# Kernel tuning notes

Measured on AMD Instinct MI355X. Metric: run time of the kernel, lower is better.

Reference implementation:

```python
import jax, jax.numpy as jnp
import numpy as np

B, N, D = 4, 4096, 1024


def setup_inputs() -> dict:
    key = jax.random.key(0)
    ks = jax.random.split(key, 7)
    s = 1.0 / np.sqrt(D)
    return {
        "x": jax.random.normal(ks[0], (B, N, D), dtype=jnp.float32),
        "Wq": jax.random.uniform(ks[1], (D, D), jnp.float32, -s, s),
        "bq": jax.random.uniform(ks[2], (D,), jnp.float32, -s, s),
        "Wk": jax.random.uniform(ks[3], (D, D), jnp.float32, -s, s),
        "bk": jax.random.uniform(ks[4], (D,), jnp.float32, -s, s),
        "Wv": jax.random.uniform(ks[5], (D, D), jnp.float32, -s, s),
        "bv": jax.random.uniform(ks[6], (D,), jnp.float32, -s, s),
    }


def reference(x, Wq, bq, Wk, bk, Wv, bv):
    # Projections (nn.Linear: x @ W.T + b; here W stored as [in, out])
    Q = x @ Wq + bq
    K = x @ Wk + bk
    V = x @ Wv + bv
    Qp = jax.nn.elu(Q) + 1.0  # positive feature map
    Kp = jax.nn.elu(K) + 1.0
    KV = jnp.einsum('bnd,bne->bde', Kp, V)          # [B, D, D]
    numerator = jnp.einsum('bnd,bde->bne', Qp, KV)  # [B, N, D]
    K_sum = Kp.sum(axis=1)                           # [B, D]
    norm = jnp.einsum('bnd,bd->bn', Qp, K_sum)[..., None]
    eps = 1e-6
    return numerator / (norm + eps)
```

## Files before the change

kernel.cpp:

```cpp
#include <hip/hip_runtime.h>
#include <hip/hip_bf16.h>
#include <cstdint>

typedef __bf16 bf16x8 __attribute__((ext_vector_type(8)));
typedef float  f32x4  __attribute__((ext_vector_type(4)));
typedef unsigned short u16x8 __attribute__((ext_vector_type(8)));

__device__ __forceinline__ unsigned short f2bf(float f) {
  __hip_bfloat16 h = __float2bfloat16(f);
  return __builtin_bit_cast(unsigned short, h);
}
__device__ __forceinline__ float bf2f(unsigned short u) {
  return __builtin_bit_cast(float, (unsigned)u << 16);
}

#define GL2LDS16(gp, lp)                                                      \
  __builtin_amdgcn_global_load_lds(                                           \
      (const __attribute__((address_space(1))) unsigned int*)(gp),            \
      (__attribute__((address_space(3))) unsigned int*)(lp), 16, 0, 0)

#define SBAR                                                                  \
  {                                                                           \
    __builtin_amdgcn_s_barrier();                                             \
    __builtin_amdgcn_sched_barrier(0);                                        \
  }
#define WAITV(n)                                                              \
  {                                                                           \
    asm volatile("s_waitcnt vmcnt(" #n ")" ::: "memory");                     \
    __builtin_amdgcn_sched_barrier(0);                                        \
  }
#define WAITL0                                                                \
  {                                                                           \
    asm volatile("s_waitcnt lgkmcnt(0)" ::: "memory");                        \
    __builtin_amdgcn_sched_barrier(0);                                        \
  }

template <int MODE>
__global__ __launch_bounds__(512, 2) void gemm256(
    const unsigned short* __restrict__ A, long long lda, long long aOffZ,
    const unsigned short* __restrict__ B, long long ldb, long long bOffZ,
    void* __restrict__ C, long long ldc, long long cOffZ,
    const float* __restrict__ bias, const float* __restrict__ norm,
    long long normOffZ, int K) {
  __shared__ __attribute__((aligned(16))) char lds[2 * 65536];
  const int t = threadIdx.x;
  const int wave = t >> 6, lane = t & 63;
  const int wm = wave >> 2, wn = wave & 3;
  const int fr = lane & 15, fq = lane >> 4;

  const int gx = gridDim.x, gy = gridDim.y;
  int flat = blockIdx.y * gx + blockIdx.x;
  const int total = gx * gy;
  if ((total & 7) == 0) flat = (flat & 7) * (total >> 3) + (flat >> 3);
  const int bx = flat % gx, by = flat / gx;
  const int m0 = by * 256, n0 = bx * 256;

  const long long z = blockIdx.z;
  long long aBase, bBase;
  if (MODE == 3) {
    const long long koff = (z & 3) * 4096 + (z >> 2) * 1024;
    aBase = koff;
    bBase = koff;
  } else if (MODE == 5) {
    aBase = (z >> 2) * 256;
    bBase = (z & 3) * 1048576ll + (z >> 2) * 256;
  } else {
    aBase = z * aOffZ;
    bBase = z * bOffZ;
  }
  const unsigned short* Az = A + aBase;
  const unsigned short* Bz = B + bBase;

  const unsigned short* gA[2];
  const unsigned short* gB[2];
#pragma unroll
  for (int c = 0; c < 2; ++c) {
    int d = c * 8192 + t * 16;
    int l = d ^ (((d >> 7) & 3) << 4);
    int row = l >> 6, kel = (l & 63) >> 1;
    gA[c] = Az + (long long)(m0 + row) * lda + kel;
    gB[c] = Bz + (long long)(n0 + row) * ldb + kel;
  }

  const int slotx = (fr >> 1) & 3;
  const int acore = wm * 8192 + fr * 64 + ((fq ^ slotx) << 4);
  const int bcore = wn * 4096 + fr * 64 + ((fq ^ slotx) << 4);

  f32x4 acc[8][4];
#pragma unroll
  for (int i = 0; i < 8; ++i)
#pragma unroll
    for (int j = 0; j < 4; ++j) acc[i][j] = (f32x4){0.f, 0.f, 0.f, 0.f};

  const int NT = K >> 6;

  auto stage_sub = [&](int tile, int which) {
    char* dst = lds + (tile & 1) * 65536 + which * 16384 + wave * 1024;
    const int kofs = (tile << 6) + ((which >> 1) << 5);
    if (which & 1) {
      GL2LDS16(gB[0] + kofs, dst);
      GL2LDS16(gB[1] + kofs, dst + 8192);
    } else {
      GL2LDS16(gA[0] + kofs, dst);
      GL2LDS16(gA[1] + kofs, dst + 8192);
    }
  };

  stage_sub(0, 0);
  stage_sub(0, 1);
  stage_sub(0, 2);
  stage_sub(0, 3);
  WAITV(4);
  SBAR;

  bf16x8 av[4], bv0[4], bv1[4];
  for (int tt = 0; tt < NT - 1; ++tt) {
    const char* bufp = lds + (tt & 1) * 65536;
#pragma unroll
    for (int i = 0; i < 4; ++i) {
      av[i] = *(const bf16x8*)(bufp + acore + i * 1024);
      bv0[i] = *(const bf16x8*)(bufp + 16384 + bcore + i * 1024);
    }
    stage_sub(tt + 1, 0);
    SBAR;
    WAITL0;
    __builtin_amdgcn_s_setprio(1);
#pragma unroll
    for (int mi = 0; mi < 4; ++mi)
#pragma unroll
      for (int ni = 0; ni < 4; ++ni)
        acc[mi][ni] = __builtin_amdgcn_mfma_f32_16x16x32_bf16(
            av[mi], bv0[ni], acc[mi][ni], 0, 0, 0);
    __builtin_amdgcn_s_setprio(0);
    SBAR;
#pragma unroll
    for (int i = 0; i < 4; ++i)
      av[i] = *(const bf16x8*)(bufp + acore + (4 + i) * 1024);
    stage_sub(tt + 1, 1);
    SBAR;
    WAITL0;
    __builtin_amdgcn_s_setprio(1);
#pragma unroll
    for (int mi = 0; mi < 4; ++mi)
#pragma unroll
      for (int ni = 0; ni < 4; ++ni)
        acc[4 + mi][ni] = __builtin_amdgcn_mfma_f32_16x16x32_bf16(
            av[mi], bv0[ni], acc[4 + mi][ni], 0, 0, 0);
    __builtin_amdgcn_s_setprio(0);
    WAITV(4);
    SBAR;
#pragma unroll
    for (int i = 0; i < 4; ++i) {
      av[i] = *(const bf16x8*)(bufp + 32768 + acore + i * 1024);
      bv1[i] = *(const bf16x8*)(bufp + 49152 + bcore + i * 1024);
    }
    stage_sub(tt + 1, 2);
    SBAR;
    WAITL0;
    __builtin_amdgcn_s_setprio(1);
#pragma unroll
    for (int mi = 0; mi < 4; ++mi)
#pragma unroll
      for (int ni = 0; ni < 4; ++ni)
        acc[mi][ni] = __builtin_amdgcn_mfma_f32_16x16x32_bf16(
            av[mi], bv1[ni], acc[mi][ni], 0, 0, 0);
    __builtin_amdgcn_s_setprio(0);
    SBAR;
#pragma unroll
    for (int i = 0; i < 4; ++i)
      av[i] = *(const bf16x8*)(bufp + 32768 + acore + (4 + i) * 1024);
    stage_sub(tt + 1, 3);
    SBAR;
    WAITL0;
    __builtin_amdgcn_s_setprio(1);
#pragma unroll
    for (int mi = 0; mi < 4; ++mi)
#pragma unroll
      for (int ni = 0; ni < 4; ++ni)
        acc[4 + mi][ni] = __builtin_amdgcn_mfma_f32_16x16x32_bf16(
            av[mi], bv1[ni], acc[4 + mi][ni], 0, 0, 0);
    __builtin_amdgcn_s_setprio(0);
    WAITV(4);
    SBAR;
  }

  {
    const char* bufp = lds + ((NT - 1) & 1) * 65536;
#pragma unroll
    for (int i = 0; i < 4; ++i) {
      av[i] = *(const bf16x8*)(bufp + acore + i * 1024);
      bv0[i] = *(const bf16x8*)(bufp + 16384 + bcore + i * 1024);
    }
    SBAR;
    WAITL0;
#pragma unroll
    for (int mi = 0; mi < 4; ++mi)
#pragma unroll
      for (int ni = 0; ni < 4; ++ni)
        acc[mi][ni] = __builtin_amdgcn_mfma_f32_16x16x32_bf16(
            av[mi], bv0[ni], acc[mi][ni], 0, 0, 0);
    SBAR;
#pragma unroll
    for (int i = 0; i < 4; ++i)
      av[i] = *(const bf16x8*)(bufp + acore + (4 + i) * 1024);
    SBAR;
    WAITL0;
#pragma unroll
    for (int mi = 0; mi < 4; ++mi)
#pragma unroll
      for (int ni = 0; ni < 4; ++ni)
        acc[4 + mi][ni] = __builtin_amdgcn_mfma_f32_16x16x32_bf16(
            av[mi], bv0[ni], acc[4 + mi][ni], 0, 0, 0);
    WAITV(0);
    SBAR;
#pragma unroll
    for (int i = 0; i < 4; ++i) {
      av[i] = *(const bf16x8*)(bufp + 32768 + acore + i * 1024);
      bv1[i] = *(const bf16x8*)(bufp + 49152 + bcore + i * 1024);
    }
    WAITL0;
#pragma unroll
    for (int mi = 0; mi < 4; ++mi)
#pragma unroll
      for (int ni = 0; ni < 4; ++ni)
        acc[mi][ni] = __builtin_amdgcn_mfma_f32_16x16x32_bf16(
            av[mi], bv1[ni], acc[mi][ni], 0, 0, 0);
#pragma unroll
    for (int i = 0; i < 4; ++i)
      av[i] = *(const bf16x8*)(bufp + 32768 + acore + (4 + i) * 1024);
    WAITL0;
#pragma unroll
    for (int mi = 0; mi < 4; ++mi)
#pragma unroll
      for (int ni = 0; ni < 4; ++ni)
        acc[4 + mi][ni] = __builtin_amdgcn_mfma_f32_16x16x32_bf16(
            av[mi], bv1[ni], acc[4 + mi][ni], 0, 0, 0);
  }

  const float* nrmz = (MODE == 4) ? (norm + z * normOffZ) : nullptr;
  float* Cf = (float*)C + z * cOffZ;
  unsigned short* Cu = (unsigned short*)C + z * cOffZ;
#pragma unroll
  for (int mi = 0; mi < 8; ++mi) {
    const int rbase = m0 + wm * 128 + mi * 16 + fq * 4;
    float nv[4];
#pragma unroll
    for (int j = 0; j < 4; ++j)
      if (MODE == 4) nv[j] = nrmz[rbase + j];
#pragma unroll
    for (int ni = 0; ni < 4; ++ni) {
      const int c = n0 + wn * 64 + ni * 16 + fr;
      float cb = 0.f;
      if (MODE == 0) cb = bias[c];
#pragma unroll
      for (int j = 0; j < 4; ++j) {
        float v = acc[mi][ni][j];
        if (MODE == 0) {
          v += cb;
          v = (v > 0.f) ? v + 1.f : __expf(v);
        }
        const long long ci = (long long)(rbase + j) * ldc + c;
        if (MODE == 4)
          Cf[ci] = v / nv[j];
        else
          Cu[ci] = f2bf(v);
      }
    }
  }
}

__global__ __launch_bounds__(256) void transpose_bf(
    const unsigned short* __restrict__ in, unsigned short* __restrict__ out) {
  __shared__ unsigned short tile[4096];
  const int t = threadIdx.x;
  const long long r0 = (long long)blockIdx.x * 64;
  const long long c0 = (long long)blockIdx.y * 64;
#pragma unroll
  for (int it = 0; it < 2; ++it) {
    const int id = it * 256 + t;
    const int r = id >> 3, cc = id & 7;
    const int pc = cc ^ ((r >> 3) & 7);
    *(u16x8*)&tile[r * 64 + pc * 8] =
        *(const u16x8*)&in[(r0 + r) * 1024 + c0 + cc * 8];
  }
  __syncthreads();
#pragma unroll
  for (int it = 0; it < 2; ++it) {
    const int id = it * 256 + t;
    const int c = id >> 3, r8 = (id & 7) * 8;
    const int pc = (c >> 3) ^ (r8 >> 3);
    u16x8 v;
#pragma unroll
    for (int j = 0; j < 8; ++j) v[j] = tile[(r8 + j) * 64 + pc * 8 + (c & 7)];
    *(u16x8*)&out[(c0 + c) * 16384 + r0 + r8] = v;
  }
}

__global__ __launch_bounds__(256) void reduce_kvt(
    const unsigned short* __restrict__ P, unsigned short* __restrict__ Out) {
  const long long i = ((long long)blockIdx.x * 256 + threadIdx.x) * 8;
  const int b = (int)(i >> 20);
  const long long ed = i & ((1ll << 20) - 1);
  float s[8] = {0.f, 0.f, 0.f, 0.f, 0.f, 0.f, 0.f, 0.f};
#pragma unroll
  for (int ks = 0; ks < 4; ++ks) {
    u16x8 v = *(const u16x8*)(P + ((long long)(ks * 4 + b) << 20) + ed);
#pragma unroll
    for (int j = 0; j < 8; ++j) s[j] += bf2f(v[j]);
  }
  u16x8 o;
#pragma unroll
  for (int j = 0; j < 8; ++j) o[j] = f2bf(s[j]);
  *(u16x8*)(Out + i) = o;
}

__global__ __launch_bounds__(256) void reduce_kvt_bias(
    const unsigned short* __restrict__ P, const float* __restrict__ bv,
    const float* __restrict__ Ksum, unsigned short* __restrict__ KVt) {
  const long long i = ((long long)blockIdx.x * 256 + threadIdx.x) * 8;
  const int b = (int)(i >> 20);
  const long long ed = i & ((1ll << 20) - 1);
  const int e = (int)(ed >> 10), d = (int)(ed & 1023);
  float s[8] = {0.f, 0.f, 0.f, 0.f, 0.f, 0.f, 0.f, 0.f};
#pragma unroll
  for (int ks = 0; ks < 4; ++ks) {
    u16x8 v = *(const u16x8*)(P + ((long long)(ks * 4 + b) << 20) + ed);
#pragma unroll
    for (int j = 0; j < 8; ++j) s[j] += bf2f(v[j]);
  }
  const float bve = bv[e];
  const float* kp = Ksum + b * 1024 + d;
  u16x8 o;
#pragma unroll
  for (int j = 0; j < 8; ++j) o[j] = f2bf(s[j] + bve * kp[j]);
  *(u16x8*)(KVt + i) = o;
}

__global__ __launch_bounds__(256) void transpose_w(
    const float* __restrict__ W, unsigned short* __restrict__ WT) {
  __shared__ float tile[32][33];
  const int tx = threadIdx.x & 31, ty = threadIdx.x >> 5;
  const int i0 = blockIdx.y * 32, o0 = blockIdx.x * 32;
#pragma unroll
  for (int s = 0; s < 32; s += 8)
    tile[ty + s][tx] = W[(long long)(i0 + ty + s) * 1024 + o0 + tx];
  __syncthreads();
#pragma unroll
  for (int s = 0; s < 32; s += 8)
    WT[(long long)(o0 + ty + s) * 1024 + i0 + tx] = f2bf(tile[tx][ty + s]);
}

__global__ __launch_bounds__(256) void convert_x(
    const float4* __restrict__ in, uint2* __restrict__ out, int n4) {
  const int stride = gridDim.x * blockDim.x;
  for (int i = blockIdx.x * blockDim.x + threadIdx.x; i < n4; i += stride) {
    float4 v = in[i];
    uint2 o;
    o.x = (unsigned)f2bf(v.x) | ((unsigned)f2bf(v.y) << 16);
    o.y = (unsigned)f2bf(v.z) | ((unsigned)f2bf(v.w) << 16);
    out[i] = o;
  }
}

__global__ __launch_bounds__(256) void ksum_kernel(
    const unsigned short* __restrict__ KpT, float* __restrict__ Ksum) {
  const int gw = (blockIdx.x * 256 + threadIdx.x) >> 6;
  const int lane = threadIdx.x & 63;
  const int d = gw >> 2, b = gw & 3;
  const unsigned short* p = KpT + (long long)d * 16384 + b * 4096 + lane * 8;
  float s = 0.f;
#pragma unroll
  for (int it = 0; it < 8; ++it) {
    u16x8 v = *(const u16x8*)(p + it * 512);
#pragma unroll
    for (int j = 0; j < 8; ++j) s += bf2f(v[j]);
  }
#pragma unroll
  for (int o = 32; o > 0; o >>= 1) s += __shfl_down(s, o, 64);
  if (lane == 0) Ksum[b * 1024 + d] = s;
}

__global__ __launch_bounds__(256) void norm_kernel(
    const unsigned short* __restrict__ Qp, const float* __restrict__ Ksum,
    float* __restrict__ nrm) {
  const int gw = (blockIdx.x * 256 + threadIdx.x) >> 6;
  const int lane = threadIdx.x & 63;
  const int b = gw >> 12;
  const unsigned short* q = Qp + (long long)gw * 1024 + lane * 8;
  const float* ks = Ksum + b * 1024 + lane * 8;
  float s = 0.f;
#pragma unroll
  for (int it = 0; it < 2; ++it) {
    u16x8 v = *(const u16x8*)(q + it * 512);
    float4 k0 = *(const float4*)(ks + it * 512);
    float4 k1 = *(const float4*)(ks + it * 512 + 4);
    s += bf2f(v[0]) * k0.x + bf2f(v[1]) * k0.y + bf2f(v[2]) * k0.z +
         bf2f(v[3]) * k0.w + bf2f(v[4]) * k1.x + bf2f(v[5]) * k1.y +
         bf2f(v[6]) * k1.z + bf2f(v[7]) * k1.w;
  }
#pragma unroll
  for (int o = 32; o > 0; o >>= 1) s += __shfl_down(s, o, 64);
  if (lane == 0) nrm[gw] = s + 1e-6f;
}

extern "C" void kernel_launch(void* const* d_in, const int* in_sizes, int n_in,
                              void* d_out, int out_size, void* d_ws,
                              size_t ws_size, hipStream_t stream) {
  const float* x  = (const float*)d_in[0];
  const float* Wq = (const float*)d_in[1];
  const float* bq = (const float*)d_in[2];
  const float* Wk = (const float*)d_in[3];
  const float* bk = (const float*)d_in[4];
  const float* Wv = (const float*)d_in[5];
  const float* bv = (const float*)d_in[6];
  float* out = (float*)d_out;

  const size_t MN = 16384ull * 1024ull;
  char* w = (char*)d_ws;
  unsigned short* R0 = (unsigned short*)w;  w += MN * 2;
  unsigned short* WT = (unsigned short*)w;  w += 3ull * 1024 * 1024 * 2;
  unsigned short* Qp = (unsigned short*)w;  w += MN * 2;
  unsigned short* R3 = (unsigned short*)w;  w += MN * 2;
  unsigned short* xbT = (unsigned short*)w;  w += MN * 2;
  unsigned short* R5 = (unsigned short*)w;  w += 4ull * 1024 * 1024 * 2;
  float* Ksum = (float*)w;  w += 4ull * 1024 * 4;
  float* nrm  = (float*)w;  w += 16384ull * 4;

  unsigned short* xb  = R0;
  unsigned short* Kp  = R3;
  unsigned short* KpT = R0;
  unsigned short* Pm  = R3;
  unsigned short* M   = R5;
  unsigned short* Pk2 = R3;
  unsigned short* KVt = R5;

  transpose_w<<<dim3(32, 32), 256, 0, stream>>>(Wq, WT);
  transpose_w<<<dim3(32, 32), 256, 0, stream>>>(Wk, WT + 1024 * 1024);
  transpose_w<<<dim3(32, 32), 256, 0, stream>>>(Wv, WT + 2 * 1024 * 1024);
  convert_x<<<2048, 256, 0, stream>>>((const float4*)x, (uint2*)xb,
                                      (int)(MN / 4));
  transpose_bf<<<dim3(256, 16), 256, 0, stream>>>(xb, xbT);

  gemm256<0><<<dim3(4, 64, 1), 512, 0, stream>>>(
      xb, 1024, 0, WT, 1024, 0, Qp, 1024, 0, bq, nullptr, 0, 1024);
  gemm256<0><<<dim3(4, 64, 1), 512, 0, stream>>>(
      xb, 1024, 0, WT + 1024 * 1024, 1024, 0, Kp, 1024, 0, bk, nullptr, 0,
      1024);
  transpose_bf<<<dim3(256, 16), 256, 0, stream>>>(Kp, KpT);
  ksum_kernel<<<1024, 256, 0, stream>>>(KpT, Ksum);
  gemm256<3><<<dim3(4, 4, 16), 512, 0, stream>>>(
      KpT, 16384, 0, xbT, 16384, 0, Pm, 1024, 1024 * 1024, nullptr, nullptr,
      0, 1024);
  reduce_kvt<<<2048, 256, 0, stream>>>(Pm, M);
  gemm256<5><<<dim3(4, 4, 16), 512, 0, stream>>>(
      WT + 2 * 1024 * 1024, 1024, 0, M, 1024, 0, Pk2, 1024, 1024 * 1024,
      nullptr, nullptr, 0, 256);
  reduce_kvt_bias<<<2048, 256, 0, stream>>>(Pk2, bv, Ksum, KVt);
  norm_kernel<<<4096, 256, 0, stream>>>(Qp, Ksum, nrm);
  gemm256<4><<<dim3(4, 16, 4), 512, 0, stream>>>(
      Qp, 1024, 4096ll * 1024, KVt, 1024, 1024 * 1024, out, 1024,
      4096ll * 1024, nullptr, nrm, 4096, 1024);
}
```

Baseline: 257.4 us.

## Shrink GEMM tile to 128x256 with triple-buffered K=32 pipeline

Replaces the 256x256 GEMM tile, which used a double-buffered 64-wide K step split into four sub-stages, with a 128x256 tile. The new tile uses 32-wide K steps staged through a three-deep LDS ring with one barrier per step. The smaller tile halves accumulator registers and LDS use, which allows four blocks per CU and doubles the grid, improving occupancy and wave count on the small GEMMs. In exchange, each block reuses data less per byte loaded and synchronises more often per unit of compute.

```diff
diff --git a/kernel.cpp b/kernel.cpp
--- a/kernel.cpp
+++ b/kernel.cpp
@@ -36,13 +36,13 @@
   }
 
 template <int MODE>
-__global__ __launch_bounds__(512, 2) void gemm256(
+__global__ __launch_bounds__(512, 4) void gemm128(
     const unsigned short* __restrict__ A, long long lda, long long aOffZ,
     const unsigned short* __restrict__ B, long long ldb, long long bOffZ,
     void* __restrict__ C, long long ldc, long long cOffZ,
     const float* __restrict__ bias, const float* __restrict__ norm,
     long long normOffZ, int K) {
-  __shared__ __attribute__((aligned(16))) char lds[2 * 65536];
+  __shared__ __attribute__((aligned(16))) char lds[3 * 24576];
   const int t = threadIdx.x;
   const int wave = t >> 6, lane = t & 63;
   const int wm = wave >> 2, wn = wave & 3;
@@ -53,7 +53,7 @@
   const int total = gx * gy;
   if ((total & 7) == 0) flat = (flat & 7) * (total >> 3) + (flat >> 3);
   const int bx = flat % gx, by = flat / gx;
-  const int m0 = by * 256, n0 = bx * 256;
+  const int m0 = by * 128, n0 = bx * 256;
 
   const long long z = blockIdx.z;
   long long aBase, bBase;
@@ -71,58 +71,54 @@
   const unsigned short* Az = A + aBase;
   const unsigned short* Bz = B + bBase;
 
-  const unsigned short* gA[2];
+  const unsigned short* gA;
   const unsigned short* gB[2];
+  {
+    int d = t * 16;
+    int l = d ^ (((d >> 7) & 3) << 4);
+    gA = Az + (long long)(m0 + (l >> 6)) * lda + ((l & 63) >> 1);
+  }
 #pragma unroll
   for (int c = 0; c < 2; ++c) {
     int d = c * 8192 + t * 16;
     int l = d ^ (((d >> 7) & 3) << 4);
-    int row = l >> 6, kel = (l & 63) >> 1;
-    gA[c] = Az + (long long)(m0 + row) * lda + kel;
-    gB[c] = Bz + (long long)(n0 + row) * ldb + kel;
+    gB[c] = Bz + (long long)(n0 + (l >> 6)) * ldb + ((l & 63) >> 1);
   }
 
   const int slotx = (fr >> 1) & 3;
-  const int acore = wm * 8192 + fr * 64 + ((fq ^ slotx) << 4);
-  const int bcore = wn * 4096 + fr * 64 + ((fq ^ slotx) << 4);
-
-  f32x4 acc[8][4];
-#pragma unroll
-  for (int i = 0; i < 8; ++i)
+  const int acore = wm * 4096 + fr * 64 + ((fq ^ slotx) << 4);
+  const int bcore = 8192 + wn * 4096 + fr * 64 + ((fq ^ slotx) << 4);
+
+  f32x4 acc[4][4];
+#pragma unroll
+  for (int i = 0; i < 4; ++i)
 #pragma unroll
     for (int j = 0; j < 4; ++j) acc[i][j] = (f32x4){0.f, 0.f, 0.f, 0.f};
 
-  const int NT = K >> 6;
-
-  auto stage_sub = [&](int tile, int which) {
-    char* dst = lds + (tile & 1) * 65536 + which * 16384 + wave * 1024;
-    const int kofs = (tile << 6) + ((which >> 1) << 5);
-    if (which & 1) {
-      GL2LDS16(gB[0] + kofs, dst);
-      GL2LDS16(gB[1] + kofs, dst + 8192);
-    } else {
-      GL2LDS16(gA[0] + kofs, dst);
-      GL2LDS16(gA[1] + kofs, dst + 8192);
+  const int NT = K >> 5;
+
+  auto stage = [&](int tile) {
+    char* sb = lds + (tile % 3) * 24576 + wave * 1024;
+    const int k0 = tile << 5;
+    GL2LDS16(gA + k0, sb);
+    GL2LDS16(gB[0] + k0, sb + 8192);
+    GL2LDS16(gB[1] + k0, sb + 16384);
+  };
+
+  stage(0);
+  stage(1);
+  WAITV(3);
+  SBAR;
+
+  bf16x8 av[4], bv[4];
+  for (int tt = 0; tt < NT - 2; ++tt) {
+    const char* sb = lds + (tt % 3) * 24576;
+    stage(tt + 2);
+#pragma unroll
+    for (int i = 0; i < 4; ++i) {
+      av[i] = *(const bf16x8*)(sb + acore + i * 1024);
+      bv[i] = *(const bf16x8*)(sb + bcore + i * 1024);
     }
-  };
-
-  stage_sub(0, 0);
-  stage_sub(0, 1);
-  stage_sub(0, 2);
-  stage_sub(0, 3);
-  WAITV(4);
-  SBAR;
-
-  bf16x8 av[4], bv0[4], bv1[4];
-  for (int tt = 0; tt < NT - 1; ++tt) {
-    const char* bufp = lds + (tt & 1) * 65536;
-#pragma unroll
-    for (int i = 0; i < 4; ++i) {
-      av[i] = *(const bf16x8*)(bufp + acore + i * 1024);
-      bv0[i] = *(const bf16x8*)(bufp + 16384 + bcore + i * 1024);
-    }
-    stage_sub(tt + 1, 0);
-    SBAR;
     WAITL0;
     __builtin_amdgcn_s_setprio(1);
 #pragma unroll
@@ -130,119 +126,51 @@
 #pragma unroll
       for (int ni = 0; ni < 4; ++ni)
         acc[mi][ni] = __builtin_amdgcn_mfma_f32_16x16x32_bf16(
-            av[mi], bv0[ni], acc[mi][ni], 0, 0, 0);
+            av[mi], bv[ni], acc[mi][ni], 0, 0, 0);
     __builtin_amdgcn_s_setprio(0);
+    WAITV(3);
     SBAR;
-#pragma unroll
-    for (int i = 0; i < 4; ++i)
-      av[i] = *(const bf16x8*)(bufp + acore + (4 + i) * 1024);
-    stage_sub(tt + 1, 1);
-    SBAR;
+  }
+
+  {
+    const char* sb = lds + ((NT - 2) % 3) * 24576;
+#pragma unroll
+    for (int i = 0; i < 4; ++i) {
+      av[i] = *(const bf16x8*)(sb + acore + i * 1024);
+      bv[i] = *(const bf16x8*)(sb + bcore + i * 1024);
+    }
     WAITL0;
-    __builtin_amdgcn_s_setprio(1);
-#pragma unroll
-    for (int mi = 0; mi < 4; ++mi)
-#pragma unroll
-      for (int ni = 0; ni < 4; ++ni)
-        acc[4 + mi][ni] = __builtin_amdgcn_mfma_f32_16x16x32_bf16(
-            av[mi], bv0[ni], acc[4 + mi][ni], 0, 0, 0);
-    __builtin_amdgcn_s_setprio(0);
-    WAITV(4);
-    SBAR;
-#pragma unroll
-    for (int i = 0; i < 4; ++i) {
-      av[i] = *(const bf16x8*)(bufp + 32768 + acore + i * 1024);
-      bv1[i] = *(const bf16x8*)(bufp + 49152 + bcore + i * 1024);
-    }
-    stage_sub(tt + 1, 2);
-    SBAR;
-    WAITL0;
-    __builtin_amdgcn_s_setprio(1);
 #pragma unroll
     for (int mi = 0; mi < 4; ++mi)
 #pragma unroll
       for (int ni = 0; ni < 4; ++ni)
         acc[mi][ni] = __builtin_amdgcn_mfma_f32_16x16x32_bf16(
-            av[mi], bv1[ni], acc[mi][ni], 0, 0, 0);
-    __builtin_amdgcn_s_setprio(0);
+            av[mi], bv[ni], acc[mi][ni], 0, 0, 0);
+    WAITV(0);
     SBAR;
-#pragma unroll
-    for (int i = 0; i < 4; ++i)
-      av[i] = *(const bf16x8*)(bufp + 32768 + acore + (4 + i) * 1024);
-    stage_sub(tt + 1, 3);
-    SBAR;
-    WAITL0;
-    __builtin_amdgcn_s_setprio(1);
-#pragma unroll
-    for (int mi = 0; mi < 4; ++mi)
-#pragma unroll
-      for (int ni = 0; ni < 4; ++ni)
-        acc[4 + mi][ni] = __builtin_amdgcn_mfma_f32_16x16x32_bf16(
-            av[mi], bv1[ni], acc[4 + mi][ni], 0, 0, 0);
-    __builtin_amdgcn_s_setprio(0);
-    WAITV(4);
-    SBAR;
-  }
-
+  }
   {
-    const char* bufp = lds + ((NT - 1) & 1) * 65536;
+    const char* sb = lds + ((NT - 1) % 3) * 24576;
 #pragma unroll
     for (int i = 0; i < 4; ++i) {
-      av[i] = *(const bf16x8*)(bufp + acore + i * 1024);
-      bv0[i] = *(const bf16x8*)(bufp + 16384 + bcore + i * 1024);
+      av[i] = *(const bf16x8*)(sb + acore + i * 1024);
+      bv[i] = *(const bf16x8*)(sb + bcore + i * 1024);
     }
-    SBAR;
     WAITL0;
 #pragma unroll
     for (int mi = 0; mi < 4; ++mi)
 #pragma unroll
       for (int ni = 0; ni < 4; ++ni)
         acc[mi][ni] = __builtin_amdgcn_mfma_f32_16x16x32_bf16(
-            av[mi], bv0[ni], acc[mi][ni], 0, 0, 0);
-    SBAR;
-#pragma unroll
-    for (int i = 0; i < 4; ++i)
-      av[i] = *(const bf16x8*)(bufp + acore + (4 + i) * 1024);
-    SBAR;
-    WAITL0;
-#pragma unroll
-    for (int mi = 0; mi < 4; ++mi)
-#pragma unroll
-      for (int ni = 0; ni < 4; ++ni)
-        acc[4 + mi][ni] = __builtin_amdgcn_mfma_f32_16x16x32_bf16(
-            av[mi], bv0[ni], acc[4 + mi][ni], 0, 0, 0);
-    WAITV(0);
-    SBAR;
-#pragma unroll
-    for (int i = 0; i < 4; ++i) {
-      av[i] = *(const bf16x8*)(bufp + 32768 + acore + i * 1024);
-      bv1[i] = *(const bf16x8*)(bufp + 49152 + bcore + i * 1024);
-    }
-    WAITL0;
-#pragma unroll
-    for (int mi = 0; mi < 4; ++mi)
-#pragma unroll
-      for (int ni = 0; ni < 4; ++ni)
-        acc[mi][ni] = __builtin_amdgcn_mfma_f32_16x16x32_bf16(
-            av[mi], bv1[ni], acc[mi][ni], 0, 0, 0);
-#pragma unroll
-    for (int i = 0; i < 4; ++i)
-      av[i] = *(const bf16x8*)(bufp + 32768 + acore + (4 + i) * 1024);
-    WAITL0;
-#pragma unroll
-    for (int mi = 0; mi < 4; ++mi)
-#pragma unroll
-      for (int ni = 0; ni < 4; ++ni)
-        acc[4 + mi][ni] = __builtin_amdgcn_mfma_f32_16x16x32_bf16(
-            av[mi], bv1[ni], acc[4 + mi][ni], 0, 0, 0);
+            av[mi], bv[ni], acc[mi][ni], 0, 0, 0);
   }
 
   const float* nrmz = (MODE == 4) ? (norm + z * normOffZ) : nullptr;
   float* Cf = (float*)C + z * cOffZ;
   unsigned short* Cu = (unsigned short*)C + z * cOffZ;
 #pragma unroll
-  for (int mi = 0; mi < 8; ++mi) {
-    const int rbase = m0 + wm * 128 + mi * 16 + fq * 4;
+  for (int mi = 0; mi < 4; ++mi) {
+    const int rbase = m0 + wm * 64 + mi * 16 + fq * 4;
     float nv[4];
 #pragma unroll
     for (int j = 0; j < 4; ++j)
@@ -421,7 +349,7 @@
   unsigned short* WT = (unsigned short*)w;  w += 3ull * 1024 * 1024 * 2;
   unsigned short* Qp = (unsigned short*)w;  w += MN * 2;
   unsigned short* R3 = (unsigned short*)w;  w += MN * 2;
-  unsigned short* xbT = (unsigned short*)w;  w += MN * 2;
+  unsigned short* xbT = (unsigned short*)w; w += MN * 2;
   unsigned short* R5 = (unsigned short*)w;  w += 4ull * 1024 * 1024 * 2;
   float* Ksum = (float*)w;  w += 4ull * 1024 * 4;
   float* nrm  = (float*)w;  w += 16384ull * 4;
@@ -441,23 +369,23 @@
                                       (int)(MN / 4));
   transpose_bf<<<dim3(256, 16), 256, 0, stream>>>(xb, xbT);
 
-  gemm256<0><<<dim3(4, 64, 1), 512, 0, stream>>>(
+  gemm128<0><<<dim3(4, 128, 1), 512, 0, stream>>>(
       xb, 1024, 0, WT, 1024, 0, Qp, 1024, 0, bq, nullptr, 0, 1024);
-  gemm256<0><<<dim3(4, 64, 1), 512, 0, stream>>>(
+  gemm128<0><<<dim3(4, 128, 1), 512, 0, stream>>>(
       xb, 1024, 0, WT + 1024 * 1024, 1024, 0, Kp, 1024, 0, bk, nullptr, 0,
       1024);
   transpose_bf<<<dim3(256, 16), 256, 0, stream>>>(Kp, KpT);
   ksum_kernel<<<1024, 256, 0, stream>>>(KpT, Ksum);
-  gemm256<3><<<dim3(4, 4, 16), 512, 0, stream>>>(
+  gemm128<3><<<dim3(4, 8, 16), 512, 0, stream>>>(
       KpT, 16384, 0, xbT, 16384, 0, Pm, 1024, 1024 * 1024, nullptr, nullptr,
       0, 1024);
   reduce_kvt<<<2048, 256, 0, stream>>>(Pm, M);
-  gemm256<5><<<dim3(4, 4, 16), 512, 0, stream>>>(
+  gemm128<5><<<dim3(4, 8, 16), 512, 0, stream>>>(
       WT + 2 * 1024 * 1024, 1024, 0, M, 1024, 0, Pk2, 1024, 1024 * 1024,
       nullptr, nullptr, 0, 256);
   reduce_kvt_bias<<<2048, 256, 0, stream>>>(Pk2, bv, Ksum, KVt);
   norm_kernel<<<4096, 256, 0, stream>>>(Qp, Ksum, nrm);
-  gemm256<4><<<dim3(4, 16, 4), 512, 0, stream>>>(
+  gemm128<4><<<dim3(4, 32, 4), 512, 0, stream>>>(
       Qp, 1024, 4096ll * 1024, KVt, 1024, 1024 * 1024, out, 1024,
       4096ll * 1024, nullptr, nrm, 4096, 1024);
 }
```

Measured after the change: 281.9 us. 1.1x slower.
